# Optimization experiments

Measured on AMD Instinct MI355X. Metric: run time of the kernel, lower is better.

The kernel has to match this reference:

```python
import jax, jax.numpy as jnp
import numpy as np
from jax import lax

DIM = 512
CODEBOOK_SIZE = 8192
B, N = 4, 2048


def setup_inputs() -> dict:
    key = jax.random.key(0)
    k1, k2, k3 = jax.random.split(key, 3)
    x = jax.random.normal(k1, (B, N, DIM), dtype=jnp.float32)
    # nn.Linear(dim, dim, bias=False) default init ~ U(-1/sqrt(dim), 1/sqrt(dim))
    bound = 1.0 / np.sqrt(DIM)
    W = jax.random.uniform(k2, (DIM, DIM), dtype=jnp.float32, minval=-bound, maxval=bound)
    codebook = jax.random.normal(k3, (CODEBOOK_SIZE, DIM), dtype=jnp.float32)
    return {"x": x, "W": W, "codebook": codebook}


def reference(x, W, codebook):
    # implicit_codebook = Linear(codebook) = codebook @ W.T   -> [C, D]
    implicit = jnp.einsum('cd,ed->ce', codebook, W)
    # nearest-codebook search (torch.cdist + argmin); argmin of L2 == argmin of
    x2 = jnp.sum(x * x, axis=-1, keepdims=True)            # [B, N, 1]
    c2 = jnp.sum(implicit * implicit, axis=-1)             # [C]
    xc = jnp.einsum('bnd,cd->bnc', x, implicit)            # [B, N, C]  (dominant cost)
    dist2 = x2 - 2.0 * xc + c2                             # [B, N, C]
    indices = jnp.argmin(dist2, axis=-1)                   # [B, N] int
    # gather codes: get_at('[c] d, b n -> b n d', ...)
    quantized = implicit[indices]                          # [B, N, D]
    # commit loss: mean of squared pairwise L2 distance, quantized detached
    commit_loss = jnp.mean(jnp.sum((x - lax.stop_gradient(quantized)) ** 2, axis=-1))
    # straight-through estimator
    quantized_out = x + lax.stop_gradient(quantized - x)
    return quantized_out, indices, commit_loss
```

## Files before the change

### kernel.cpp

```cpp
#include <hip/hip_runtime.h>
#include <stdint.h>

#define DIM   512
#define CBSZ  8192
#define BN    8192
#define LDSS  132

#define LOSC  4096.0f
#define LOSCI (1.0f/4096.0f)
#define BK    64

typedef _Float16 f16x8 __attribute__((ext_vector_type(8)));
typedef _Float16 f16x4 __attribute__((ext_vector_type(4)));
typedef float    f32x4 __attribute__((ext_vector_type(4)));

__device__ __forceinline__ unsigned int fkey(float v) {
  unsigned int u = __float_as_uint(v);
  return (u & 0x80000000u) ? ~u : (u | 0x80000000u);
}

__device__ __forceinline__ void gload16(const void* g, void* l) {
  __builtin_amdgcn_global_load_lds(
      (const __attribute__((address_space(1))) void*)g,
      (__attribute__((address_space(3))) void*)l, 16, 0, 0);
}

__global__ __launch_bounds__(256) void k_split(
    const float* __restrict__ in, _Float16* __restrict__ hi,
    _Float16* __restrict__ lo) {
  const int t = blockIdx.x * 256 + threadIdx.x;
  const float4* p = (const float4*)in + (size_t)t * 2;
  float4 v0 = p[0], v1 = p[1];
  float vv[8] = {v0.x, v0.y, v0.z, v0.w, v1.x, v1.y, v1.z, v1.w};
  f16x8 h, l;
#pragma unroll
  for (int j = 0; j < 8; ++j) {
    h[j] = (_Float16)vv[j];
    l[j] = (_Float16)((vv[j] - (float)h[j]) * LOSC);
  }
  *(f16x8*)(hi + (size_t)t * 8) = h;
  *(f16x8*)(lo + (size_t)t * 8) = l;
}

__global__ __launch_bounds__(256) void k_implicit(
    const float* __restrict__ cb, const float* __restrict__ Wm,
    float* __restrict__ imp, _Float16* __restrict__ imph,
    _Float16* __restrict__ impl, float* __restrict__ c2) {
  __shared__ float As[32][LDSS];
  __shared__ float Bs[32][LDSS];
  const int t  = threadIdx.x;
  const int tx = t & 15, ty = t >> 4;
  const int tm0 = blockIdx.x * 128;
  const int tn0 = blockIdx.y * 128;
  float acc[8][8];
#pragma unroll
  for (int i = 0; i < 8; ++i)
#pragma unroll
    for (int j = 0; j < 8; ++j) acc[i][j] = 0.f;

  const int chunk = t & 7, row0 = t >> 3;
  for (int kt = 0; kt < DIM; kt += 32) {
#pragma unroll
    for (int rr = 0; rr < 4; ++rr) {
      int row = row0 + rr * 32;
      float4 av = *(const float4*)(cb + (size_t)(tm0 + row) * DIM + kt + chunk * 4);
      float4 bv = *(const float4*)(Wm + (size_t)(tn0 + row) * DIM + kt + chunk * 4);
      As[chunk*4+0][row] = av.x; As[chunk*4+1][row] = av.y;
      As[chunk*4+2][row] = av.z; As[chunk*4+3][row] = av.w;
      Bs[chunk*4+0][row] = bv.x; Bs[chunk*4+1][row] = bv.y;
      Bs[chunk*4+2][row] = bv.z; Bs[chunk*4+3][row] = bv.w;
    }
    __syncthreads();
#pragma unroll
    for (int k = 0; k < 32; ++k) {
      float4 a0 = *(const float4*)&As[k][ty * 4];
      float4 a1 = *(const float4*)&As[k][64 + ty * 4];
      float4 b0 = *(const float4*)&Bs[k][tx * 4];
      float4 b1 = *(const float4*)&Bs[k][64 + tx * 4];
      float av[8] = {a0.x, a0.y, a0.z, a0.w, a1.x, a1.y, a1.z, a1.w};
      float bv[8] = {b0.x, b0.y, b0.z, b0.w, b1.x, b1.y, b1.z, b1.w};
#pragma unroll
      for (int i = 0; i < 8; ++i)
#pragma unroll
        for (int j = 0; j < 8; ++j) acc[i][j] = fmaf(av[i], bv[j], acc[i][j]);
    }
    __syncthreads();
  }
#pragma unroll
  for (int i = 0; i < 8; ++i) {
    int rl = ((i >> 2) << 6) + ty * 4 + (i & 3);
    int rg = tm0 + rl;
    float s = 0.f;
#pragma unroll
    for (int jh = 0; jh < 2; ++jh) {
      float4 v = make_float4(acc[i][jh*4+0], acc[i][jh*4+1], acc[i][jh*4+2], acc[i][jh*4+3]);
      int cg = tn0 + (jh << 6) + tx * 4;
      *(float4*)(imp + (size_t)rg * DIM + cg) = v;
      float vs[4] = {v.x, v.y, v.z, v.w};
      f16x4 vh, vl;
#pragma unroll
      for (int q = 0; q < 4; ++q) {
        vh[q] = (_Float16)vs[q];
        vl[q] = (_Float16)((vs[q] - (float)vh[q]) * LOSC);
      }
      *(f16x4*)(imph + (size_t)rg * DIM + cg) = vh;
      *(f16x4*)(impl + (size_t)rg * DIM + cg) = vl;
      s += v.x*v.x + v.y*v.y + v.z*v.z + v.w*v.w;
    }
    atomicAdd(&c2[rg], s);
  }
}

__global__ __launch_bounds__(256, 2) void k_argmin(
    const _Float16* __restrict__ xh, const _Float16* __restrict__ xl,
    const _Float16* __restrict__ ch, const _Float16* __restrict__ cl,
    const float* __restrict__ c2, unsigned long long* __restrict__ best) {
  __shared__ _Float16 As[128 * 128];
  __shared__ _Float16 Bs[128 * 128];
  const int t    = threadIdx.x;
  const int lane = t & 63, w = t >> 6;
  const int wm = w >> 1, wn = w & 1;
  const int fr = lane & 15, fq = lane >> 4;
  const int tm0 = blockIdx.x * 128;
  const int tn0 = blockIdx.y * 128;

  f32x4 ahh[4][4], axx[4][4];
#pragma unroll
  for (int i = 0; i < 4; ++i)
#pragma unroll
    for (int j = 0; j < 4; ++j) {
      ahh[i][j] = (f32x4){0.f, 0.f, 0.f, 0.f};
      axx[i][j] = (f32x4){0.f, 0.f, 0.f, 0.f};
    }

  const int sBase = (lane & 15) ^ (lane >> 4);
  const int rIn   = lane >> 4;
  char* As_b = (char*)As;
  char* Bs_b = (char*)Bs;

  int rAoff[4], rBoff[4];
#pragma unroll
  for (int i = 0; i < 4; ++i) {
    rAoff[i] = (wm * 64 + i * 16 + fr) * 256 + ((fq ^ fr) << 4);
    rBoff[i] = (wn * 64 + i * 16 + fr) * 256 + ((fq ^ fr) << 4);
  }

  for (int kt = 0; kt < DIM; kt += BK) {
    __syncthreads();
#pragma unroll
    for (int q = 0; q < 8; ++q) {
      const int s    = sBase ^ ((q & 3) << 2);
      const int row  = w * 32 + q * 4 + rIn;
      const int koff = (s >> 3) * 32 + (s & 3) * 8;
      const _Float16* pa =
          ((s & 4) ? xl : xh) + (size_t)(tm0 + row) * DIM + kt + koff;
      const _Float16* pb =
          ((s & 4) ? cl : ch) + (size_t)(tn0 + row) * DIM + kt + koff;
      gload16(pa, As_b + (w * 32 + q * 4) * 256);
      gload16(pb, Bs_b + (w * 32 + q * 4) * 256);
    }
    __syncthreads();

#pragma unroll
    for (int kk = 0; kk < 2; ++kk) {
      const int kx = kk << 7;
      f16x8 bh[4], bl[4];
#pragma unroll
      for (int j = 0; j < 4; ++j) {
        bh[j] = *(const f16x8*)(Bs_b + (rBoff[j] ^ kx));
        bl[j] = *(const f16x8*)(Bs_b + (rBoff[j] ^ kx ^ 64));
      }
#pragma unroll
      for (int i = 0; i < 4; ++i) {
        f16x8 ah = *(const f16x8*)(As_b + (rAoff[i] ^ kx));
        f16x8 al = *(const f16x8*)(As_b + (rAoff[i] ^ kx ^ 64));
#pragma unroll
        for (int j = 0; j < 4; ++j) {
          ahh[i][j] = __builtin_amdgcn_mfma_f32_16x16x32_f16(ah, bh[j], ahh[i][j], 0, 0, 0);
          axx[i][j] = __builtin_amdgcn_mfma_f32_16x16x32_f16(ah, bl[j], axx[i][j], 0, 0, 0);
          axx[i][j] = __builtin_amdgcn_mfma_f32_16x16x32_f16(al, bh[j], axx[i][j], 0, 0, 0);
        }
      }
    }
  }

  float c2v[4];
  int   cgv[4];
#pragma unroll
  for (int j = 0; j < 4; ++j) {
    cgv[j] = tn0 + wn * 64 + j * 16 + fr;
    c2v[j] = c2[cgv[j]];
  }
  unsigned long long rmin[4][4];
#pragma unroll
  for (int i = 0; i < 4; ++i)
#pragma unroll
    for (int q = 0; q < 4; ++q) {
      unsigned long long m = ~0ull;
#pragma unroll
      for (int j = 0; j < 4; ++j) {
        float v = c2v[j] - 2.0f * (ahh[i][j][q] + axx[i][j][q] * LOSCI);
        unsigned long long p =
            ((unsigned long long)fkey(v) << 32) | (unsigned int)cgv[j];
        if (p < m) m = p;
      }
#pragma unroll
      for (int d = 1; d < 16; d <<= 1) {
        unsigned long long o = __shfl_xor(m, d, 64);
        if (o < m) m = o;
      }
      rmin[i][q] = m;
    }
  __syncthreads();
  unsigned long long* red = (unsigned long long*)As;
  if (fr == 0) {
#pragma unroll
    for (int i = 0; i < 4; ++i)
#pragma unroll
      for (int q = 0; q < 4; ++q)
        red[wn * 128 + wm * 64 + i * 16 + fq * 4 + q] = rmin[i][q];
  }
  __syncthreads();
  if (t < 128) {
    unsigned long long a = red[t], b = red[128 + t];
    if (b < a) a = b;
    atomicMin(&best[tm0 + t], a);
  }
}

__global__ __launch_bounds__(256) void k_gather(
    const float* __restrict__ x, const float* __restrict__ imp,
    const unsigned long long* __restrict__ best,
    float* __restrict__ out_q, float* __restrict__ out_idx,
    float* __restrict__ out_loss) {
  __shared__ float part[4];
  const int wave = threadIdx.x >> 6;
  const int lane = threadIdx.x & 63;
  float s = 0.f;
#pragma unroll
  for (int rr = 0; rr < 4; ++rr) {
    const int r = blockIdx.x * 16 + wave * 4 + rr;
    const unsigned long long p = best[r];
    const int idx = (int)(p & 0xffffffffu);
    const float4* xr = (const float4*)(x   + (size_t)r   * DIM);
    const float4* qr = (const float4*)(imp + (size_t)idx * DIM);
    float4*       o  = (float4*)(out_q + (size_t)r * DIM);
#pragma unroll
    for (int jh = 0; jh < 2; ++jh) {
      float4 xv = xr[lane + jh * 64];
      float4 qv = qr[lane + jh * 64];
      float4 ov;
      ov.x = xv.x + (qv.x - xv.x);  ov.y = xv.y + (qv.y - xv.y);
      ov.z = xv.z + (qv.z - xv.z);  ov.w = xv.w + (qv.w - xv.w);
      o[lane + jh * 64] = ov;
      float dx = xv.x - qv.x, dy = xv.y - qv.y, dz = xv.z - qv.z, dw = xv.w - qv.w;
      s += dx*dx + dy*dy + dz*dz + dw*dw;
    }
    if (lane == 0) out_idx[r] = (float)idx;
  }
#pragma unroll
  for (int off = 32; off > 0; off >>= 1) s += __shfl_down(s, off);
  if (lane == 0) part[wave] = s;
  __syncthreads();
  if (threadIdx.x == 0) {
    float tot = (part[0] + part[1]) + (part[2] + part[3]);
    atomicAdd(out_loss, tot * (1.0f / (float)BN));
  }
}

extern "C" void kernel_launch(void* const* d_in, const int* in_sizes, int n_in,
                              void* d_out, int out_size, void* d_ws, size_t ws_size,
                              hipStream_t stream) {
  const float* x  = (const float*)d_in[0];
  const float* Wm = (const float*)d_in[1];
  const float* cb = (const float*)d_in[2];

  float* out   = (float*)d_out;
  float* out_q = out;
  float* out_i = out + (size_t)BN * DIM;
  float* out_l = out + (size_t)BN * DIM + BN;

  char* ws = (char*)d_ws;
  float* imp = (float*)ws;
  float* c2  = (float*)(ws + 16777216);
  unsigned long long* best = (unsigned long long*)(ws + 16777216 + 32768);
  _Float16* xh = (_Float16*)(ws + 16875520);
  _Float16* xl = (_Float16*)(ws + 16875520 + 8388608);
  _Float16* ih = (_Float16*)(ws + 16875520 + 2 * 8388608);
  _Float16* il = (_Float16*)(ws + 16875520 + 3 * 8388608);

  hipMemsetAsync(c2, 0, CBSZ * sizeof(float), stream);
  hipMemsetAsync(best, 0xFF, CBSZ * sizeof(unsigned long long), stream);
  hipMemsetAsync(out_l, 0, sizeof(float), stream);

  k_split<<<(BN * DIM / 8) / 256, 256, 0, stream>>>(x, xh, xl);

  dim3 gA(CBSZ / 128, DIM / 128);
  k_implicit<<<gA, 256, 0, stream>>>(cb, Wm, imp, ih, il, c2);

  dim3 gB(BN / 128, CBSZ / 128);
  k_argmin<<<gB, 256, 0, stream>>>(xh, xl, ih, il, c2, best);

  k_gather<<<BN / 16, 256, 0, stream>>>(x, imp, best, out_q, out_i, out_l);
}
```

Before: 386.0 us.

## Compute implicit codebook with split-fp16 MFMA instead of scalar FP32 FMA

The implicit codebook GEMM (codebook @ W^T) moves from a scalar FP32 register-tiled kernel to an MFMA kernel using the same hi/lo fp16 split scheme as the argmin kernel. Codebook and W are first split into fp16 hi/lo pairs by extra k_split launches and loaded into swizzled LDS with global_load_lds. The goal is to replace the FP32 FMA throughput cost of this 4 GFLOP GEMM with matrix-core throughput, paying for two extra split passes and extra workspace. Precision is kept close to FP32 through three MFMA products per step (hh, hl, lh), and c2 is reduced with a cross-lane shuffle before the atomic add.

Result: faster. 336.3 us (-12.9%).

```diff
diff --git a/kernel.cpp b/kernel.cpp
--- a/kernel.cpp
+++ b/kernel.cpp
@@ -4,14 +4,12 @@
 #define DIM   512
 #define CBSZ  8192
 #define BN    8192
-#define LDSS  132
 
 #define LOSC  4096.0f
 #define LOSCI (1.0f/4096.0f)
 #define BK    64
 
 typedef _Float16 f16x8 __attribute__((ext_vector_type(8)));
-typedef _Float16 f16x4 __attribute__((ext_vector_type(4)));
 typedef float    f32x4 __attribute__((ext_vector_type(4)));
 
 __device__ __forceinline__ unsigned int fkey(float v) {
@@ -42,72 +40,101 @@
   *(f16x8*)(lo + (size_t)t * 8) = l;
 }
 
-__global__ __launch_bounds__(256) void k_implicit(
-    const float* __restrict__ cb, const float* __restrict__ Wm,
+__global__ __launch_bounds__(256, 2) void k_implicit(
+    const _Float16* __restrict__ cbh, const _Float16* __restrict__ cbl,
+    const _Float16* __restrict__ Wh,  const _Float16* __restrict__ Wl,
     float* __restrict__ imp, _Float16* __restrict__ imph,
     _Float16* __restrict__ impl, float* __restrict__ c2) {
-  __shared__ float As[32][LDSS];
-  __shared__ float Bs[32][LDSS];
-  const int t  = threadIdx.x;
-  const int tx = t & 15, ty = t >> 4;
+  __shared__ _Float16 As[128 * 128];
+  __shared__ _Float16 Bs[128 * 128];
+  const int t    = threadIdx.x;
+  const int lane = t & 63, w = t >> 6;
+  const int wm = w >> 1, wn = w & 1;
+  const int fr = lane & 15, fq = lane >> 4;
   const int tm0 = blockIdx.x * 128;
   const int tn0 = blockIdx.y * 128;
-  float acc[8][8];
-#pragma unroll
-  for (int i = 0; i < 8; ++i)
-#pragma unroll
-    for (int j = 0; j < 8; ++j) acc[i][j] = 0.f;
-
-  const int chunk = t & 7, row0 = t >> 3;
-  for (int kt = 0; kt < DIM; kt += 32) {
-#pragma unroll
-    for (int rr = 0; rr < 4; ++rr) {
-      int row = row0 + rr * 32;
-      float4 av = *(const float4*)(cb + (size_t)(tm0 + row) * DIM + kt + chunk * 4);
-      float4 bv = *(const float4*)(Wm + (size_t)(tn0 + row) * DIM + kt + chunk * 4);
-      As[chunk*4+0][row] = av.x; As[chunk*4+1][row] = av.y;
-      As[chunk*4+2][row] = av.z; As[chunk*4+3][row] = av.w;
-      Bs[chunk*4+0][row] = bv.x; Bs[chunk*4+1][row] = bv.y;
-      Bs[chunk*4+2][row] = bv.z; Bs[chunk*4+3][row] = bv.w;
-    }
+
+  f32x4 ahh[4][4], axx[4][4];
+#pragma unroll
+  for (int i = 0; i < 4; ++i)
+#pragma unroll
+    for (int j = 0; j < 4; ++j) {
+      ahh[i][j] = (f32x4){0.f, 0.f, 0.f, 0.f};
+      axx[i][j] = (f32x4){0.f, 0.f, 0.f, 0.f};
+    }
+
+  const int sBase = (lane & 15) ^ (lane >> 4);
+  const int rIn   = lane >> 4;
+  char* As_b = (char*)As;
+  char* Bs_b = (char*)Bs;
+
+  int rAoff[4], rBoff[4];
+#pragma unroll
+  for (int i = 0; i < 4; ++i) {
+    rAoff[i] = (wm * 64 + i * 16 + fr) * 256 + ((fq ^ fr) << 4);
+    rBoff[i] = (wn * 64 + i * 16 + fr) * 256 + ((fq ^ fr) << 4);
+  }
+
+  for (int kt = 0; kt < DIM; kt += BK) {
     __syncthreads();
 #pragma unroll
-    for (int k = 0; k < 32; ++k) {
-      float4 a0 = *(const float4*)&As[k][ty * 4];
-      float4 a1 = *(const float4*)&As[k][64 + ty * 4];
-      float4 b0 = *(const float4*)&Bs[k][tx * 4];
-      float4 b1 = *(const float4*)&Bs[k][64 + tx * 4];
-      float av[8] = {a0.x, a0.y, a0.z, a0.w, a1.x, a1.y, a1.z, a1.w};
-      float bv[8] = {b0.x, b0.y, b0.z, b0.w, b1.x, b1.y, b1.z, b1.w};
-#pragma unroll
-      for (int i = 0; i < 8; ++i)
-#pragma unroll
-        for (int j = 0; j < 8; ++j) acc[i][j] = fmaf(av[i], bv[j], acc[i][j]);
+    for (int q = 0; q < 8; ++q) {
+      const int s    = sBase ^ ((q & 3) << 2);
+      const int row  = w * 32 + q * 4 + rIn;
+      const int koff = (s >> 3) * 32 + (s & 3) * 8;
+      const _Float16* pa =
+          ((s & 4) ? cbl : cbh) + (size_t)(tm0 + row) * DIM + kt + koff;
+      const _Float16* pb =
+          ((s & 4) ? Wl : Wh) + (size_t)(tn0 + row) * DIM + kt + koff;
+      gload16(pa, As_b + (w * 32 + q * 4) * 256);
+      gload16(pb, Bs_b + (w * 32 + q * 4) * 256);
     }
     __syncthreads();
-  }
-#pragma unroll
-  for (int i = 0; i < 8; ++i) {
-    int rl = ((i >> 2) << 6) + ty * 4 + (i & 3);
-    int rg = tm0 + rl;
-    float s = 0.f;
-#pragma unroll
-    for (int jh = 0; jh < 2; ++jh) {
-      float4 v = make_float4(acc[i][jh*4+0], acc[i][jh*4+1], acc[i][jh*4+2], acc[i][jh*4+3]);
-      int cg = tn0 + (jh << 6) + tx * 4;
-      *(float4*)(imp + (size_t)rg * DIM + cg) = v;
-      float vs[4] = {v.x, v.y, v.z, v.w};
-      f16x4 vh, vl;
-#pragma unroll
-      for (int q = 0; q < 4; ++q) {
-        vh[q] = (_Float16)vs[q];
-        vl[q] = (_Float16)((vs[q] - (float)vh[q]) * LOSC);
-      }
-      *(f16x4*)(imph + (size_t)rg * DIM + cg) = vh;
-      *(f16x4*)(impl + (size_t)rg * DIM + cg) = vl;
-      s += v.x*v.x + v.y*v.y + v.z*v.z + v.w*v.w;
-    }
-    atomicAdd(&c2[rg], s);
+
+#pragma unroll
+    for (int kk = 0; kk < 2; ++kk) {
+      const int kx = kk << 7;
+      f16x8 bh[4], bl[4];
+#pragma unroll
+      for (int j = 0; j < 4; ++j) {
+        bh[j] = *(const f16x8*)(Bs_b + (rBoff[j] ^ kx));
+        bl[j] = *(const f16x8*)(Bs_b + (rBoff[j] ^ kx ^ 64));
+      }
+#pragma unroll
+      for (int i = 0; i < 4; ++i) {
+        f16x8 ah = *(const f16x8*)(As_b + (rAoff[i] ^ kx));
+        f16x8 al = *(const f16x8*)(As_b + (rAoff[i] ^ kx ^ 64));
+#pragma unroll
+        for (int j = 0; j < 4; ++j) {
+          ahh[i][j] = __builtin_amdgcn_mfma_f32_16x16x32_f16(ah, bh[j], ahh[i][j], 0, 0, 0);
+          axx[i][j] = __builtin_amdgcn_mfma_f32_16x16x32_f16(ah, bl[j], axx[i][j], 0, 0, 0);
+          axx[i][j] = __builtin_amdgcn_mfma_f32_16x16x32_f16(al, bh[j], axx[i][j], 0, 0, 0);
+        }
+      }
+    }
+  }
+
+#pragma unroll
+  for (int i = 0; i < 4; ++i) {
+#pragma unroll
+    for (int q = 0; q < 4; ++q) {
+      const int rg = tm0 + wm * 64 + i * 16 + fq * 4 + q;
+      float s2 = 0.f;
+#pragma unroll
+      for (int j = 0; j < 4; ++j) {
+        const int cg = tn0 + wn * 64 + j * 16 + fr;
+        float val = ahh[i][j][q] + axx[i][j][q] * LOSCI;
+        imp[(size_t)rg * DIM + cg] = val;
+        _Float16 vh = (_Float16)val;
+        _Float16 vl = (_Float16)((val - (float)vh) * LOSC);
+        imph[(size_t)rg * DIM + cg] = vh;
+        impl[(size_t)rg * DIM + cg] = vl;
+        s2 += val * val;
+      }
+#pragma unroll
+      for (int d = 1; d < 16; d <<= 1) s2 += __shfl_xor(s2, d, 64);
+      if (fr == 0) atomicAdd(&c2[rg], s2);
+    }
   }
 }
 
@@ -283,20 +310,26 @@
   char* ws = (char*)d_ws;
   float* imp = (float*)ws;
   float* c2  = (float*)(ws + 16777216);
-  unsigned long long* best = (unsigned long long*)(ws + 16777216 + 32768);
-  _Float16* xh = (_Float16*)(ws + 16875520);
-  _Float16* xl = (_Float16*)(ws + 16875520 + 8388608);
-  _Float16* ih = (_Float16*)(ws + 16875520 + 2 * 8388608);
-  _Float16* il = (_Float16*)(ws + 16875520 + 3 * 8388608);
+  unsigned long long* best = (unsigned long long*)(ws + 16809984);
+  _Float16* xh  = (_Float16*)(ws + 16875520);
+  _Float16* xl  = (_Float16*)(ws + 16875520 + 1 * 8388608);
+  _Float16* ih  = (_Float16*)(ws + 16875520 + 2 * 8388608);
+  _Float16* il  = (_Float16*)(ws + 16875520 + 3 * 8388608);
+  _Float16* cbh = (_Float16*)(ws + 16875520 + 4 * 8388608);
+  _Float16* cbl = (_Float16*)(ws + 16875520 + 5 * 8388608);
+  _Float16* Wh  = (_Float16*)(ws + 16875520 + 6 * 8388608);
+  _Float16* Wl  = (_Float16*)(ws + 16875520 + 6 * 8388608 + 524288);
 
   hipMemsetAsync(c2, 0, CBSZ * sizeof(float), stream);
   hipMemsetAsync(best, 0xFF, CBSZ * sizeof(unsigned long long), stream);
   hipMemsetAsync(out_l, 0, sizeof(float), stream);
 
   k_split<<<(BN * DIM / 8) / 256, 256, 0, stream>>>(x, xh, xl);
+  k_split<<<(CBSZ * DIM / 8) / 256, 256, 0, stream>>>(cb, cbh, cbl);
+  k_split<<<(DIM * DIM / 8) / 256, 256, 0, stream>>>(Wm, Wh, Wl);
 
   dim3 gA(CBSZ / 128, DIM / 128);
-  k_implicit<<<gA, 256, 0, stream>>>(cb, Wm, imp, ih, il, c2);
+  k_implicit<<<gA, 256, 0, stream>>>(cbh, cbl, Wh, Wl, imp, ih, il, c2);
 
   dim3 gB(BN / 128, CBSZ / 128);
   k_argmin<<<gB, 256, 0, stream>>>(xh, xl, ih, il, c2, best);
```
